# Optimization experiments

Hardware: AMD Instinct MI355X
Metric: run time of the kernel (lower is better)

Reference implementation:

```python
import jax, jax.numpy as jnp
import numpy as np

B, S, H = 2, 1024, 2048
NH, NKV, HD = 32, 8, 64          # head_dim = H // NH
G = NH // NKV                    # GQA group size = 4
THETA = 500000.0
EPS = 1e-5
SCALE = HD ** -0.5


def _rope_neox(x, positions):
    # x: [B, S, n_heads, HD]; neox style: rotate concatenated halves
    inv_freq = 1.0 / (THETA ** (jnp.arange(0, HD, 2, dtype=jnp.float32) / HD))  # [HD/2]
    ang = positions[..., None].astype(jnp.float32) * inv_freq                    # [B, S, HD/2]
    cos = jnp.cos(ang)[:, :, None, :]
    sin = jnp.sin(ang)[:, :, None, :]
    x1, x2 = jnp.split(x, 2, axis=-1)
    return jnp.concatenate([x1 * cos - x2 * sin, x2 * cos + x1 * sin], axis=-1)


def setup_inputs() -> dict:
    key = jax.random.key(0)
    k1, k2, k3 = jax.random.split(key, 3)
    hidden_states = jax.random.normal(k1, (B, S, H), jnp.float32)
    w_qkv = jax.random.normal(k2, ((NH + 2 * NKV) * HD, H), jnp.float32) * 0.02
    w_o = jax.random.normal(k3, (H, NH * HD), jnp.float32) * 0.02
    norm_w = jnp.ones((H,), jnp.float32)
    positions = jnp.broadcast_to(jnp.arange(S, dtype=jnp.int32), (B, S))
    return {"hidden_states": hidden_states, "positions": positions,
            "w_qkv": w_qkv, "w_o": w_o, "norm_w": norm_w}


def reference(hidden_states, positions, w_qkv, w_o, norm_w):
    # QKV projection (bias=False) and split
    qkv = hidden_states @ w_qkv.T                                 # [B,S,3072]
    q, k, v = jnp.split(qkv, [NH * HD, NH * HD + NKV * HD], axis=-1)
    q = q.reshape(B, S, NH, HD)
    k = k.reshape(B, S, NKV, HD)
    v = v.reshape(B, S, NKV, HD)

    # RoPE on q and k (full rotary_dim = head_dim)
    q = _rope_neox(q, positions)
    k = _rope_neox(k, positions)

    # Causal GQA attention (dense-prefill equivalent of RadixAttention)
    qg = q.reshape(B, S, NKV, G, HD)
    scores = jnp.einsum('bqhgd,bkhd->bhgqk', qg, k) * SCALE       # [B,NKV,G,S,S]
    causal = jnp.tril(jnp.ones((S, S), dtype=bool))
    scores = jnp.where(causal, scores, jnp.float32(-1e30))
    probs = jax.nn.softmax(scores, axis=-1)
    attn = jnp.einsum('bhgqk,bkhd->bqhgd', probs, v).reshape(B, S, NH * HD)

    # BitNet sub-norm (RMSNorm) then output projection
    var = jnp.mean(attn * attn, axis=-1, keepdims=True)
    normed = attn * jax.lax.rsqrt(var + EPS) * norm_w
    return normed @ w_o.T                                         # [B,S,H]
```

## Files before the change

kernel.cpp:

```cpp
#include <hip/hip_runtime.h>
#include <hip/hip_bf16.h>
#include <cstdint>
#include <cstddef>

typedef __bf16 bf16;
typedef __bf16 bf16x4 __attribute__((ext_vector_type(4)));
typedef __bf16 bf16x8 __attribute__((ext_vector_type(8)));
typedef float  f32x4  __attribute__((ext_vector_type(4)));

__device__ __forceinline__ void async_copy16(const void* g, void* l) {
  __builtin_amdgcn_global_load_lds((const __attribute__((address_space(1))) void*)g,
                                   (__attribute__((address_space(3))) void*)l,
                                   16, 0, 0);
}

__global__ void detect_dtype(const unsigned int* __restrict__ w, int* __restrict__ flag) {
  const int t = threadIdx.x;
  int weird = 0;
#pragma unroll
  for (int c = 0; c < 2; ++c) {
    const unsigned int lo = w[c * 64 + t] & 0xffffu;
    const unsigned int ex = (lo >> 7) & 0xffu;
    if (ex >= 134u) ++weird;
  }
  const unsigned long long m1 = __ballot(weird >= 1);
  const unsigned long long m2 = __ballot(weird == 2);
  if (t == 0) *flag = (__popcll(m1) + __popcll(m2) >= 8) ? 1 : 0;
}

__global__ __launch_bounds__(256) void convert_all(
    const void* __restrict__ s0, const void* __restrict__ s1,
    const void* __restrict__ s2, const void* __restrict__ s3,
    bf16* __restrict__ d0, bf16* __restrict__ d1,
    bf16* __restrict__ d2, bf16* __restrict__ d3,
    const int* __restrict__ flag) {
  const int i = blockIdx.x * 256 + threadIdx.x;
  if (i >= 3670528) return;
  const void* src; bf16* dst; int off;
  if      (i < 1048576) { src = s0; dst = d0; off = i; }
  else if (i < 2621440) { src = s1; dst = d1; off = i - 1048576; }
  else if (i < 3670016) { src = s2; dst = d2; off = i - 2621440; }
  else                  { src = s3; dst = d3; off = i - 3670016; }
  bf16x4 o;
  if (*flag) {
    const float4 v = ((const float4*)src)[off];
    o[0] = (bf16)v.x; o[1] = (bf16)v.y; o[2] = (bf16)v.z; o[3] = (bf16)v.w;
  } else {
    o = ((const bf16x4*)src)[off];
  }
  *(bf16x4*)(dst + (size_t)off * 4) = o;
}

__global__ __launch_bounds__(256) void gemm_qkv_rope(
    const bf16* __restrict__ A, const bf16* __restrict__ B,
    const int* __restrict__ pos,
    bf16* __restrict__ Q, bf16* __restrict__ K, bf16* __restrict__ V)
{
  __shared__ __align__(16) bf16 As[64 * 32];
  __shared__ __align__(16) bf16 Bs[128 * 32];
  const int tid = threadIdx.x, wave = tid >> 6, lane = tid & 63;
  const int l15 = lane & 15, l4 = lane >> 4;
  const int m0 = blockIdx.y * 64, n0 = blockIdx.x * 128;
  const int wm = (wave >> 1) * 32, wn = (wave & 1) * 64;
  const int KD = 2048;

  f32x4 acc[2][4] = {};

  const int ea = tid * 8;
  const int rowa = ea >> 5, ka = ea & 31;
  const bf16* Aa  = A + (size_t)(m0 + rowa) * KD + ka;
  const bf16* Bb0 = B + (size_t)(n0 + rowa) * KD + ka;
  const bf16* Bb1 = B + (size_t)(n0 + 64 + rowa) * KD + ka;

  for (int kt = 0; kt < KD; kt += 32) {
    async_copy16(Aa  + kt, As + ea);
    async_copy16(Bb0 + kt, Bs + ea);
    async_copy16(Bb1 + kt, Bs + 2048 + ea);
    __syncthreads();
    bf16x8 af[2], bfr[4];
#pragma unroll
    for (int i = 0; i < 2; ++i)
      af[i] = *(const bf16x8*)(As + (wm + i * 16 + l15) * 32 + l4 * 8);
#pragma unroll
    for (int j = 0; j < 4; ++j)
      bfr[j] = *(const bf16x8*)(Bs + (wn + j * 16 + l15) * 32 + l4 * 8);
#pragma unroll
    for (int i = 0; i < 2; ++i)
#pragma unroll
      for (int j = 0; j < 4; ++j)
        acc[i][j] = __builtin_amdgcn_mfma_f32_16x16x32_bf16(af[i], bfr[j], acc[i][j], 0, 0, 0);
    __syncthreads();
  }

  if (n0 < 2560) {
    const bool isQ = (n0 < 2048);
#pragma unroll
    for (int i = 0; i < 2; ++i)
#pragma unroll
      for (int j = 0; j < 4; ++j) {
        const int col = n0 + wn + j * 16 + l15;
        const int hd = isQ ? col : (col - 2048);
        const int hh = hd >> 6, d = hd & 63;
        const int fi = d & 31;
        const float ifr = __expf((float)fi * -0.41007385554f);
#pragma unroll
        for (int r = 0; r < 4; ++r) {
          const int m = m0 + wm + i * 16 + l4 * 4 + r;
          const int b = m >> 10, s = m & 1023;
          const float ang = (float)pos[m] * ifr;
          float sn, cs;
          sincosf(ang, &sn, &cs);
          const float x  = acc[i][j][r];
          const float xp = acc[i][j ^ 2][r];
          const float v = (d < 32) ? (x * cs - xp * sn) : (x * cs + xp * sn);
          if (isQ) Q[(((size_t)(b * 32 + hh)) * 1024 + s) * 64 + d] = (bf16)(v * 0.125f);
          else     K[(((size_t)(b * 8 + hh)) * 1024 + s) * 64 + d] = (bf16)v;
        }
      }
  } else {
#pragma unroll
    for (int i = 0; i < 2; ++i)
#pragma unroll
      for (int j = 0; j < 4; ++j) {
        const int cv = n0 + wn + j * 16 + l15 - 2560;
        const int hh = cv >> 6, d = cv & 63;
#pragma unroll
        for (int r = 0; r < 4; ++r) {
          const int m = m0 + wm + i * 16 + l4 * 4 + r;
          const int b = m >> 10, s = m & 1023;
          V[(((size_t)(b * 8 + hh)) * 64 + d) * 1024 + s] = (bf16)acc[i][j][r];
        }
      }
  }
}

__global__ __launch_bounds__(256) void attn_kernel(
    const bf16* __restrict__ Q, const bf16* __restrict__ K,
    const bf16* __restrict__ Vt, bf16* __restrict__ O)
{
  __shared__ __align__(16) bf16 Ks[2 * 128 * 32];
  __shared__ __align__(16) bf16 Vs[4 * 64 * 32];
  __shared__ __align__(16) bf16 Ps[4 * 128 * 40];

  const int tid = threadIdx.x, wave = tid >> 6, lane = tid & 63;
  const int l15 = lane & 15, l4 = lane >> 4;
  const int ip = blockIdx.x, bh = blockIdx.y;
  const int b = bh >> 5, h = bh & 31, kvh = h >> 2;
  const int qlo = ip * 64, qhi = (15 - ip) * 64;
  const bf16* Qb = Q + ((size_t)(b * 32 + h)) * 65536;
  const bf16* Kb = K + ((size_t)(b * 8 + kvh)) * 65536;
  const bf16* Vb = Vt + ((size_t)(b * 8 + kvh)) * 65536;

#pragma unroll
  for (int c = 0; c < 4; ++c) {
    const int e = c * 2048 + tid * 8;
    const int dchunk = e >> 12;
    const int row = (e & 4095) >> 5;
    const int qb = (row < 64) ? qlo : qhi;
    async_copy16(Qb + (size_t)(qb + (row & 63)) * 64 + dchunk * 32 + (e & 31), Ps + e);
  }
  __syncthreads();
  bf16x8 aq[2][2];
#pragma unroll
  for (int i = 0; i < 2; ++i)
#pragma unroll
    for (int s = 0; s < 2; ++s)
      aq[i][s] = *(const bf16x8*)(Ps + s * 4096 + (i * 64 + wave * 16 + l15) * 32 + l4 * 8);
  __syncthreads();

  float m_s[2][4], l_s[2][4];
  f32x4 o_acc[2][4] = {};
#pragma unroll
  for (int i = 0; i < 2; ++i)
#pragma unroll
    for (int r = 0; r < 4; ++r) { m_s[i][r] = -3.0e4f; l_s[i][r] = 0.f; }

  const int nkt = (1151 - 64 * ip) >> 7;
  for (int kt = 0; kt < nkt; ++kt) {
    const int k0 = kt * 128;
    const bool lo_act = (k0 < (ip + 1) * 64);
#pragma unroll
    for (int c = 0; c < 4; ++c) {
      const int e = c * 2048 + tid * 8;
      const int dchunk = e >> 12;
      const int krow = (e & 4095) >> 5;
      async_copy16(Kb + (size_t)(k0 + krow) * 64 + dchunk * 32 + (e & 31), Ks + e);
      const int kc = e >> 11;
      const int drow = (e & 2047) >> 5;
      async_copy16(Vb + (size_t)drow * 1024 + k0 + kc * 32 + (e & 31), Vs + e);
    }
    __syncthreads();

    f32x4 sc[2][8] = {};
#pragma unroll
    for (int j = 0; j < 8; ++j) {
      const bf16x8 bk0 = *(const bf16x8*)(Ks + (j * 16 + l15) * 32 + l4 * 8);
      const bf16x8 bk1 = *(const bf16x8*)(Ks + 4096 + (j * 16 + l15) * 32 + l4 * 8);
      sc[1][j] = __builtin_amdgcn_mfma_f32_16x16x32_bf16(aq[1][0], bk0, sc[1][j], 0, 0, 0);
      sc[1][j] = __builtin_amdgcn_mfma_f32_16x16x32_bf16(aq[1][1], bk1, sc[1][j], 0, 0, 0);
      if (lo_act) {
        sc[0][j] = __builtin_amdgcn_mfma_f32_16x16x32_bf16(aq[0][0], bk0, sc[0][j], 0, 0, 0);
        sc[0][j] = __builtin_amdgcn_mfma_f32_16x16x32_bf16(aq[0][1], bk1, sc[0][j], 0, 0, 0);
      }
    }

#pragma unroll
    for (int hh = 0; hh < 2; ++hh) {
      if (hh == 0 && !lo_act) continue;
      const int qb = hh ? qhi : qlo;
#pragma unroll
      for (int r = 0; r < 4; ++r) {
        const int rl = wave * 16 + l4 * 4 + r;
        const int rg = qb + rl;
        float mx = -3.0e4f;
#pragma unroll
        for (int j = 0; j < 8; ++j) {
          float v = sc[hh][j][r];
          if (k0 + j * 16 + l15 > rg) v = -3.0e4f;
          sc[hh][j][r] = v;
          mx = fmaxf(mx, v);
        }
#pragma unroll
        for (int off = 1; off < 16; off <<= 1) mx = fmaxf(mx, __shfl_xor(mx, off));
        const float mnew = fmaxf(m_s[hh][r], mx);
        const float alpha = __expf(m_s[hh][r] - mnew);
        m_s[hh][r] = mnew;
        float rs = 0.f;
#pragma unroll
        for (int j = 0; j < 8; ++j) {
          const float pv = __expf(sc[hh][j][r] - mnew);
          rs += pv;
          Ps[(j >> 1) * 5120 + (hh * 64 + rl) * 40 + (j & 1) * 16 + l15] = (bf16)pv;
        }
#pragma unroll
        for (int off = 1; off < 16; off <<= 1) rs += __shfl_xor(rs, off);
        l_s[hh][r] = l_s[hh][r] * alpha + rs;
#pragma unroll
        for (int jd = 0; jd < 4; ++jd) o_acc[hh][jd][r] *= alpha;
      }
    }
    __syncthreads();

#pragma unroll
    for (int ks = 0; ks < 4; ++ks) {
      bf16x8 bv[4];
#pragma unroll
      for (int jd = 0; jd < 4; ++jd)
        bv[jd] = *(const bf16x8*)(Vs + ks * 2048 + (jd * 16 + l15) * 32 + l4 * 8);
#pragma unroll
      for (int hh = 0; hh < 2; ++hh) {
        if (hh == 0 && !lo_act) continue;
        const bf16x8 ap = *(const bf16x8*)(Ps + ks * 5120 + (hh * 64 + wave * 16 + l15) * 40 + l4 * 8);
#pragma unroll
        for (int jd = 0; jd < 4; ++jd)
          o_acc[hh][jd] = __builtin_amdgcn_mfma_f32_16x16x32_bf16(ap, bv[jd], o_acc[hh][jd], 0, 0, 0);
      }
    }
    __syncthreads();
  }

#pragma unroll
  for (int hh = 0; hh < 2; ++hh) {
    const int qb = hh ? qhi : qlo;
#pragma unroll
    for (int r = 0; r < 4; ++r) {
      const float inv = 1.0f / l_s[hh][r];
      const int srow = qb + wave * 16 + l4 * 4 + r;
      bf16* op = O + ((size_t)(b * 1024 + srow)) * 2048 + h * 64;
#pragma unroll
      for (int jd = 0; jd < 4; ++jd)
        op[jd * 16 + l15] = (bf16)(o_acc[hh][jd][r] * inv);
    }
  }
}

__global__ __launch_bounds__(256) void rmsnorm(
    const bf16* __restrict__ X, const bf16* __restrict__ W, bf16* __restrict__ Y)
{
  const int row = blockIdx.x;
  const int tid = threadIdx.x, wave = tid >> 6, lane = tid & 63;
  const bf16* xr = X + (size_t)row * 2048;
  const int base = tid * 8;
  const bf16x8 xv = *(const bf16x8*)(xr + base);
  float ss = 0.f;
  float xf[8];
#pragma unroll
  for (int j = 0; j < 8; ++j) { xf[j] = (float)xv[j]; ss += xf[j] * xf[j]; }
#pragma unroll
  for (int off = 32; off > 0; off >>= 1) ss += __shfl_xor(ss, off);
  __shared__ float red[4];
  if (lane == 0) red[wave] = ss;
  __syncthreads();
  const float tot = red[0] + red[1] + red[2] + red[3];
  const float rinv = rsqrtf(tot * (1.0f / 2048.0f) + 1e-5f);
  const bf16x8 wv = *(const bf16x8*)(W + base);
  bf16x8 yv;
#pragma unroll
  for (int j = 0; j < 8; ++j) yv[j] = (bf16)(xf[j] * rinv * (float)wv[j]);
  *(bf16x8*)(Y + (size_t)row * 2048 + base) = yv;
}

__global__ __launch_bounds__(256) void gemm_out(
    const bf16* __restrict__ A, const bf16* __restrict__ B,
    void* __restrict__ out, const int* __restrict__ flag)
{
  __shared__ __align__(16) bf16 As[64 * 32];
  __shared__ __align__(16) bf16 Bs[128 * 32];
  const int tid = threadIdx.x, wave = tid >> 6, lane = tid & 63;
  const int l15 = lane & 15, l4 = lane >> 4;
  const int m0 = blockIdx.y * 64, n0 = blockIdx.x * 128;
  const int wm = (wave >> 1) * 32, wn = (wave & 1) * 64;
  const int KD = 2048;

  f32x4 acc[2][4] = {};

  const int ea = tid * 8;
  const int rowa = ea >> 5, ka = ea & 31;
  const bf16* Aa  = A + (size_t)(m0 + rowa) * KD + ka;
  const bf16* Bb0 = B + (size_t)(n0 + rowa) * KD + ka;
  const bf16* Bb1 = B + (size_t)(n0 + 64 + rowa) * KD + ka;

  for (int kt = 0; kt < KD; kt += 32) {
    async_copy16(Aa  + kt, As + ea);
    async_copy16(Bb0 + kt, Bs + ea);
    async_copy16(Bb1 + kt, Bs + 2048 + ea);
    __syncthreads();
    bf16x8 af[2], bfr[4];
#pragma unroll
    for (int i = 0; i < 2; ++i)
      af[i] = *(const bf16x8*)(As + (wm + i * 16 + l15) * 32 + l4 * 8);
#pragma unroll
    for (int j = 0; j < 4; ++j)
      bfr[j] = *(const bf16x8*)(Bs + (wn + j * 16 + l15) * 32 + l4 * 8);
#pragma unroll
    for (int i = 0; i < 2; ++i)
#pragma unroll
      for (int j = 0; j < 4; ++j)
        acc[i][j] = __builtin_amdgcn_mfma_f32_16x16x32_bf16(af[i], bfr[j], acc[i][j], 0, 0, 0);
    __syncthreads();
  }

  const bool f32out = (*flag != 0);
#pragma unroll
  for (int i = 0; i < 2; ++i)
#pragma unroll
    for (int j = 0; j < 4; ++j) {
      const int col = n0 + wn + j * 16 + l15;
#pragma unroll
      for (int r = 0; r < 4; ++r) {
        const size_t idx = (size_t)(m0 + wm + i * 16 + l4 * 4 + r) * 2048 + col;
        if (f32out) ((float*)out)[idx] = acc[i][j][r];
        else        ((bf16*)out)[idx]  = (bf16)acc[i][j][r];
      }
    }
}

extern "C" void kernel_launch(void* const* d_in, const int* in_sizes, int n_in,
                              void* d_out, int out_size, void* d_ws, size_t ws_size,
                              hipStream_t stream) {
  const void* hs     = d_in[0];
  const int*  pos    = (const int*)d_in[1];
  const void* w_qkv  = d_in[2];
  const void* w_o    = d_in[3];
  const void* norm_w = d_in[4];

  char* ws = (char*)d_ws;
  bf16* hs_b    = (bf16*)(ws);
  bf16* wqkv_b  = (bf16*)(ws + 8388608);
  bf16* w_o_b   = (bf16*)(ws + 20971520);
  bf16* normw_b = (bf16*)(ws + 29360128);
  int*  flag    = (int*) (ws + 29364224);
  bf16* Qr      = (bf16*)(ws + 29364288);
  bf16* Kr      = (bf16*)(ws + 37752896);
  bf16* Vtr     = (bf16*)(ws + 39850048);
  bf16* attn_o  = (bf16*)(ws + 41947200);
  bf16* normed  = hs_b;

  detect_dtype<<<1, 64, 0, stream>>>((const unsigned int*)hs, flag);
  convert_all<<<14338, 256, 0, stream>>>(hs, w_qkv, w_o, norm_w,
                                         hs_b, wqkv_b, w_o_b, normw_b, flag);

  gemm_qkv_rope<<<dim3(24, 32), 256, 0, stream>>>(hs_b, wqkv_b, pos, Qr, Kr, Vtr);
  attn_kernel<<<dim3(8, 64), 256, 0, stream>>>(Qr, Kr, Vtr, attn_o);
  rmsnorm<<<2048, 256, 0, stream>>>(attn_o, normw_b, normed);
  gemm_out<<<dim3(16, 32), 256, 0, stream>>>(normed, w_o_b, d_out, flag);
}
```

Measured before the change: 225.9 us.

## Fuse RMSNorm into attention epilogue and output GEMM, widen GEMM k-step

Removes the standalone RMSNorm pass. Attention now accumulates per-row sums of squares with atomics, a tiny kernel turns them into reciprocal RMS values, the norm weight is folded into w_o during conversion, and the output GEMM scales rows in its epilogue. Both GEMMs now load 64-wide K tiles per barrier, halving the number of syncs, and RoPE uses the fast __sincosf intrinsic. The cost is atomic traffic, an extra launch, twice the LDS per GEMM block, and slightly different rounding because the normalization is applied after the matmul instead of to bf16 activations.

Measured after the change: 213.1 us. -5.7%, faster.

```diff
diff --git a/kernel.cpp b/kernel.cpp
--- a/kernel.cpp
+++ b/kernel.cpp
@@ -14,40 +14,58 @@
                                    16, 0, 0);
 }
 
-__global__ void detect_dtype(const unsigned int* __restrict__ w, int* __restrict__ flag) {
+__global__ __launch_bounds__(256) void detect_dtype(
+    const unsigned int* __restrict__ w, int* __restrict__ flag,
+    float* __restrict__ ssum) {
   const int t = threadIdx.x;
-  int weird = 0;
-#pragma unroll
-  for (int c = 0; c < 2; ++c) {
-    const unsigned int lo = w[c * 64 + t] & 0xffffu;
-    const unsigned int ex = (lo >> 7) & 0xffu;
-    if (ex >= 134u) ++weird;
-  }
-  const unsigned long long m1 = __ballot(weird >= 1);
-  const unsigned long long m2 = __ballot(weird == 2);
-  if (t == 0) *flag = (__popcll(m1) + __popcll(m2) >= 8) ? 1 : 0;
+  ((float4*)ssum)[t * 2]     = make_float4(0.f, 0.f, 0.f, 0.f);
+  ((float4*)ssum)[t * 2 + 1] = make_float4(0.f, 0.f, 0.f, 0.f);
+  if (t < 64) {
+    int weird = 0;
+#pragma unroll
+    for (int c = 0; c < 2; ++c) {
+      const unsigned int lo = w[c * 64 + t] & 0xffffu;
+      const unsigned int ex = (lo >> 7) & 0xffu;
+      if (ex >= 134u) ++weird;
+    }
+    const unsigned long long m1 = __ballot(weird >= 1);
+    const unsigned long long m2 = __ballot(weird == 2);
+    if (t == 0) *flag = (__popcll(m1) + __popcll(m2) >= 8) ? 1 : 0;
+  }
 }
 
 __global__ __launch_bounds__(256) void convert_all(
     const void* __restrict__ s0, const void* __restrict__ s1,
     const void* __restrict__ s2, const void* __restrict__ s3,
-    bf16* __restrict__ d0, bf16* __restrict__ d1,
-    bf16* __restrict__ d2, bf16* __restrict__ d3,
+    bf16* __restrict__ d0, bf16* __restrict__ d1, bf16* __restrict__ d2,
     const int* __restrict__ flag) {
   const int i = blockIdx.x * 256 + threadIdx.x;
-  if (i >= 3670528) return;
-  const void* src; bf16* dst; int off;
+  if (i >= 3670016) return;
+  const bool f32 = (*flag != 0);
+  const void* src; bf16* dst; int off; bool fold = false;
   if      (i < 1048576) { src = s0; dst = d0; off = i; }
   else if (i < 2621440) { src = s1; dst = d1; off = i - 1048576; }
-  else if (i < 3670016) { src = s2; dst = d2; off = i - 2621440; }
-  else                  { src = s3; dst = d3; off = i - 3670016; }
+  else                  { src = s2; dst = d2; off = i - 2621440; fold = true; }
+  float v[4];
+  if (f32) {
+    const float4 t = ((const float4*)src)[off];
+    v[0] = t.x; v[1] = t.y; v[2] = t.z; v[3] = t.w;
+  } else {
+    const bf16x4 t = ((const bf16x4*)src)[off];
+#pragma unroll
+    for (int j = 0; j < 4; ++j) v[j] = (float)t[j];
+  }
+  if (fold) {
+    const int k0 = (off * 4) & 2047;
+#pragma unroll
+    for (int j = 0; j < 4; ++j) {
+      const float w = f32 ? ((const float*)s3)[k0 + j] : (float)((const bf16*)s3)[k0 + j];
+      v[j] *= w;
+    }
+  }
   bf16x4 o;
-  if (*flag) {
-    const float4 v = ((const float4*)src)[off];
-    o[0] = (bf16)v.x; o[1] = (bf16)v.y; o[2] = (bf16)v.z; o[3] = (bf16)v.w;
-  } else {
-    o = ((const bf16x4*)src)[off];
-  }
+#pragma unroll
+  for (int j = 0; j < 4; ++j) o[j] = (bf16)v[j];
   *(bf16x4*)(dst + (size_t)off * 4) = o;
 }
 
@@ -56,8 +74,8 @@
     const int* __restrict__ pos,
     bf16* __restrict__ Q, bf16* __restrict__ K, bf16* __restrict__ V)
 {
-  __shared__ __align__(16) bf16 As[64 * 32];
-  __shared__ __align__(16) bf16 Bs[128 * 32];
+  __shared__ __align__(16) bf16 As[2 * 64 * 32];
+  __shared__ __align__(16) bf16 Bs[2 * 128 * 32];
   const int tid = threadIdx.x, wave = tid >> 6, lane = tid & 63;
   const int l15 = lane & 15, l4 = lane >> 4;
   const int m0 = blockIdx.y * 64, n0 = blockIdx.x * 128;
@@ -66,29 +84,35 @@
 
   f32x4 acc[2][4] = {};
 
-  const int ea = tid * 8;
-  const int rowa = ea >> 5, ka = ea & 31;
-  const bf16* Aa  = A + (size_t)(m0 + rowa) * KD + ka;
-  const bf16* Bb0 = B + (size_t)(n0 + rowa) * KD + ka;
-  const bf16* Bb1 = B + (size_t)(n0 + 64 + rowa) * KD + ka;
-
-  for (int kt = 0; kt < KD; kt += 32) {
-    async_copy16(Aa  + kt, As + ea);
-    async_copy16(Bb0 + kt, Bs + ea);
-    async_copy16(Bb1 + kt, Bs + 2048 + ea);
-    __syncthreads();
-    bf16x8 af[2], bfr[4];
-#pragma unroll
-    for (int i = 0; i < 2; ++i)
-      af[i] = *(const bf16x8*)(As + (wm + i * 16 + l15) * 32 + l4 * 8);
-#pragma unroll
-    for (int j = 0; j < 4; ++j)
-      bfr[j] = *(const bf16x8*)(Bs + (wn + j * 16 + l15) * 32 + l4 * 8);
-#pragma unroll
-    for (int i = 0; i < 2; ++i)
+  for (int kt = 0; kt < KD; kt += 64) {
+#pragma unroll
+    for (int c = 0; c < 2; ++c) {
+      const int e = c * 2048 + tid * 8;
+      const int row = (e >> 5) & 63, kc = e >> 11, o = e & 31;
+      async_copy16(A + (size_t)(m0 + row) * KD + kt + kc * 32 + o, As + e);
+    }
+#pragma unroll
+    for (int c = 0; c < 4; ++c) {
+      const int e = c * 2048 + tid * 8;
+      const int row = (e >> 5) & 127, kc = e >> 12, o = e & 31;
+      async_copy16(B + (size_t)(n0 + row) * KD + kt + kc * 32 + o, Bs + e);
+    }
+    __syncthreads();
+#pragma unroll
+    for (int s = 0; s < 2; ++s) {
+      bf16x8 af[2], bfr[4];
+#pragma unroll
+      for (int i = 0; i < 2; ++i)
+        af[i] = *(const bf16x8*)(As + s * 2048 + (wm + i * 16 + l15) * 32 + l4 * 8);
 #pragma unroll
       for (int j = 0; j < 4; ++j)
-        acc[i][j] = __builtin_amdgcn_mfma_f32_16x16x32_bf16(af[i], bfr[j], acc[i][j], 0, 0, 0);
+        bfr[j] = *(const bf16x8*)(Bs + s * 4096 + (wn + j * 16 + l15) * 32 + l4 * 8);
+#pragma unroll
+      for (int i = 0; i < 2; ++i)
+#pragma unroll
+        for (int j = 0; j < 4; ++j)
+          acc[i][j] = __builtin_amdgcn_mfma_f32_16x16x32_bf16(af[i], bfr[j], acc[i][j], 0, 0, 0);
+    }
     __syncthreads();
   }
 
@@ -109,7 +133,7 @@
           const int b = m >> 10, s = m & 1023;
           const float ang = (float)pos[m] * ifr;
           float sn, cs;
-          sincosf(ang, &sn, &cs);
+          __sincosf(ang, &sn, &cs);
           const float x  = acc[i][j][r];
           const float xp = acc[i][j ^ 2][r];
           const float v = (d < 32) ? (x * cs - xp * sn) : (x * cs + xp * sn);
@@ -136,7 +160,7 @@
 
 __global__ __launch_bounds__(256) void attn_kernel(
     const bf16* __restrict__ Q, const bf16* __restrict__ K,
-    const bf16* __restrict__ Vt, bf16* __restrict__ O)
+    const bf16* __restrict__ Vt, bf16* __restrict__ O, float* __restrict__ ssum)
 {
   __shared__ __align__(16) bf16 Ks[2 * 128 * 32];
   __shared__ __align__(16) bf16 Vs[4 * 64 * 32];
@@ -267,45 +291,33 @@
       const float inv = 1.0f / l_s[hh][r];
       const int srow = qb + wave * 16 + l4 * 4 + r;
       bf16* op = O + ((size_t)(b * 1024 + srow)) * 2048 + h * 64;
-#pragma unroll
-      for (int jd = 0; jd < 4; ++jd)
-        op[jd * 16 + l15] = (bf16)(o_acc[hh][jd][r] * inv);
-    }
-  }
-}
-
-__global__ __launch_bounds__(256) void rmsnorm(
-    const bf16* __restrict__ X, const bf16* __restrict__ W, bf16* __restrict__ Y)
-{
-  const int row = blockIdx.x;
-  const int tid = threadIdx.x, wave = tid >> 6, lane = tid & 63;
-  const bf16* xr = X + (size_t)row * 2048;
-  const int base = tid * 8;
-  const bf16x8 xv = *(const bf16x8*)(xr + base);
-  float ss = 0.f;
-  float xf[8];
-#pragma unroll
-  for (int j = 0; j < 8; ++j) { xf[j] = (float)xv[j]; ss += xf[j] * xf[j]; }
-#pragma unroll
-  for (int off = 32; off > 0; off >>= 1) ss += __shfl_xor(ss, off);
-  __shared__ float red[4];
-  if (lane == 0) red[wave] = ss;
-  __syncthreads();
-  const float tot = red[0] + red[1] + red[2] + red[3];
-  const float rinv = rsqrtf(tot * (1.0f / 2048.0f) + 1e-5f);
-  const bf16x8 wv = *(const bf16x8*)(W + base);
-  bf16x8 yv;
-#pragma unroll
-  for (int j = 0; j < 8; ++j) yv[j] = (bf16)(xf[j] * rinv * (float)wv[j]);
-  *(bf16x8*)(Y + (size_t)row * 2048 + base) = yv;
+      float ss = 0.f;
+#pragma unroll
+      for (int jd = 0; jd < 4; ++jd) {
+        const float v = o_acc[hh][jd][r] * inv;
+        op[jd * 16 + l15] = (bf16)v;
+        ss += v * v;
+      }
+#pragma unroll
+      for (int off = 1; off < 16; off <<= 1) ss += __shfl_xor(ss, off);
+      if (l15 == 0) atomicAdd(&ssum[b * 1024 + srow], ss);
+    }
+  }
+}
+
+__global__ __launch_bounds__(256) void rsqrt_rows(
+    const float* __restrict__ ssum, float* __restrict__ rinv) {
+  const int i = blockIdx.x * 256 + threadIdx.x;
+  if (i < 2048) rinv[i] = rsqrtf(ssum[i] * (1.0f / 2048.0f) + 1e-5f);
 }
 
 __global__ __launch_bounds__(256) void gemm_out(
     const bf16* __restrict__ A, const bf16* __restrict__ B,
+    const float* __restrict__ rinv,
     void* __restrict__ out, const int* __restrict__ flag)
 {
-  __shared__ __align__(16) bf16 As[64 * 32];
-  __shared__ __align__(16) bf16 Bs[128 * 32];
+  __shared__ __align__(16) bf16 As[2 * 64 * 32];
+  __shared__ __align__(16) bf16 Bs[2 * 128 * 32];
   const int tid = threadIdx.x, wave = tid >> 6, lane = tid & 63;
   const int l15 = lane & 15, l4 = lane >> 4;
   const int m0 = blockIdx.y * 64, n0 = blockIdx.x * 128;
@@ -314,29 +326,35 @@
 
   f32x4 acc[2][4] = {};
 
-  const int ea = tid * 8;
-  const int rowa = ea >> 5, ka = ea & 31;
-  const bf16* Aa  = A + (size_t)(m0 + rowa) * KD + ka;
-  const bf16* Bb0 = B + (size_t)(n0 + rowa) * KD + ka;
-  const bf16* Bb1 = B + (size_t)(n0 + 64 + rowa) * KD + ka;
-
-  for (int kt = 0; kt < KD; kt += 32) {
-    async_copy16(Aa  + kt, As + ea);
-    async_copy16(Bb0 + kt, Bs + ea);
-    async_copy16(Bb1 + kt, Bs + 2048 + ea);
-    __syncthreads();
-    bf16x8 af[2], bfr[4];
-#pragma unroll
-    for (int i = 0; i < 2; ++i)
-      af[i] = *(const bf16x8*)(As + (wm + i * 16 + l15) * 32 + l4 * 8);
-#pragma unroll
-    for (int j = 0; j < 4; ++j)
-      bfr[j] = *(const bf16x8*)(Bs + (wn + j * 16 + l15) * 32 + l4 * 8);
-#pragma unroll
-    for (int i = 0; i < 2; ++i)
+  for (int kt = 0; kt < KD; kt += 64) {
+#pragma unroll
+    for (int c = 0; c < 2; ++c) {
+      const int e = c * 2048 + tid * 8;
+      const int row = (e >> 5) & 63, kc = e >> 11, o = e & 31;
+      async_copy16(A + (size_t)(m0 + row) * KD + kt + kc * 32 + o, As + e);
+    }
+#pragma unroll
+    for (int c = 0; c < 4; ++c) {
+      const int e = c * 2048 + tid * 8;
+      const int row = (e >> 5) & 127, kc = e >> 12, o = e & 31;
+      async_copy16(B + (size_t)(n0 + row) * KD + kt + kc * 32 + o, Bs + e);
+    }
+    __syncthreads();
+#pragma unroll
+    for (int s = 0; s < 2; ++s) {
+      bf16x8 af[2], bfr[4];
+#pragma unroll
+      for (int i = 0; i < 2; ++i)
+        af[i] = *(const bf16x8*)(As + s * 2048 + (wm + i * 16 + l15) * 32 + l4 * 8);
 #pragma unroll
       for (int j = 0; j < 4; ++j)
-        acc[i][j] = __builtin_amdgcn_mfma_f32_16x16x32_bf16(af[i], bfr[j], acc[i][j], 0, 0, 0);
+        bfr[j] = *(const bf16x8*)(Bs + s * 4096 + (wn + j * 16 + l15) * 32 + l4 * 8);
+#pragma unroll
+      for (int i = 0; i < 2; ++i)
+#pragma unroll
+        for (int j = 0; j < 4; ++j)
+          acc[i][j] = __builtin_amdgcn_mfma_f32_16x16x32_bf16(af[i], bfr[j], acc[i][j], 0, 0, 0);
+    }
     __syncthreads();
   }
 
@@ -344,13 +362,16 @@
 #pragma unroll
   for (int i = 0; i < 2; ++i)
 #pragma unroll
-    for (int j = 0; j < 4; ++j) {
-      const int col = n0 + wn + j * 16 + l15;
-#pragma unroll
-      for (int r = 0; r < 4; ++r) {
-        const size_t idx = (size_t)(m0 + wm + i * 16 + l4 * 4 + r) * 2048 + col;
-        if (f32out) ((float*)out)[idx] = acc[i][j][r];
-        else        ((bf16*)out)[idx]  = (bf16)acc[i][j][r];
+    for (int r = 0; r < 4; ++r) {
+      const int row = m0 + wm + i * 16 + l4 * 4 + r;
+      const float ri = rinv[row];
+#pragma unroll
+      for (int j = 0; j < 4; ++j) {
+        const int col = n0 + wn + j * 16 + l15;
+        const size_t idx = (size_t)row * 2048 + col;
+        const float v = ri * acc[i][j][r];
+        if (f32out) ((float*)out)[idx] = v;
+        else        ((bf16*)out)[idx]  = (bf16)v;
       }
     }
 }
@@ -365,23 +386,23 @@
   const void* norm_w = d_in[4];
 
   char* ws = (char*)d_ws;
-  bf16* hs_b    = (bf16*)(ws);
-  bf16* wqkv_b  = (bf16*)(ws + 8388608);
-  bf16* w_o_b   = (bf16*)(ws + 20971520);
-  bf16* normw_b = (bf16*)(ws + 29360128);
-  int*  flag    = (int*) (ws + 29364224);
-  bf16* Qr      = (bf16*)(ws + 29364288);
-  bf16* Kr      = (bf16*)(ws + 37752896);
-  bf16* Vtr     = (bf16*)(ws + 39850048);
-  bf16* attn_o  = (bf16*)(ws + 41947200);
-  bf16* normed  = hs_b;
-
-  detect_dtype<<<1, 64, 0, stream>>>((const unsigned int*)hs, flag);
-  convert_all<<<14338, 256, 0, stream>>>(hs, w_qkv, w_o, norm_w,
-                                         hs_b, wqkv_b, w_o_b, normw_b, flag);
+  bf16*  hs_b   = (bf16*) (ws);
+  bf16*  wqkv_b = (bf16*) (ws + 8388608);
+  bf16*  w_o_b  = (bf16*) (ws + 20971520);
+  int*   flag   = (int*)  (ws + 29360128);
+  float* ssum   = (float*)(ws + 29360192);
+  bf16*  Qr     = (bf16*) (ws + 29368384);
+  bf16*  Kr     = (bf16*) (ws + 37756992);
+  bf16*  Vtr    = (bf16*) (ws + 39854144);
+  bf16*  attn_o = (bf16*) (ws + 41951296);
+  float* rinv   = (float*)(ws + 50339904);
+
+  detect_dtype<<<1, 256, 0, stream>>>((const unsigned int*)hs, flag, ssum);
+  convert_all<<<14336, 256, 0, stream>>>(hs, w_qkv, w_o, norm_w,
+                                         hs_b, wqkv_b, w_o_b, flag);
 
   gemm_qkv_rope<<<dim3(24, 32), 256, 0, stream>>>(hs_b, wqkv_b, pos, Qr, Kr, Vtr);
-  attn_kernel<<<dim3(8, 64), 256, 0, stream>>>(Qr, Kr, Vtr, attn_o);
-  rmsnorm<<<2048, 256, 0, stream>>>(attn_o, normw_b, normed);
-  gemm_out<<<dim3(16, 32), 256, 0, stream>>>(normed, w_o_b, d_out, flag);
-}
+  attn_kernel<<<dim3(8, 64), 256, 0, stream>>>(Qr, Kr, Vtr, attn_o, ssum);
+  rsqrt_rows<<<8, 256, 0, stream>>>(ssum, rinv);
+  gemm_out<<<dim3(16, 32), 256, 0, stream>>>(attn_o, w_o_b, rinv, d_out, flag);
+}
```
